# Optimization experiments

Hardware: AMD Instinct MI355X
Metric: run time of the kernel (lower is better)

## Reference

```python
import jax, jax.numpy as jnp
import numpy as np

N = 100_000      # nodes
E = 1_200_000    # edges (before self-loops)
F_IN = 128       # num_node_features
G = 256          # number of graphs in the batch
C = 10           # num_classes
NEG_SLOPE = 0.2  # PyG GATConv default


def setup_inputs() -> dict:
    key = jax.random.key(0)
    ks = jax.random.split(key, 20)
    x = jax.random.normal(ks[0], (N, F_IN), jnp.float32)
    edge_index = jax.random.randint(ks[1], (2, E), 0, N, dtype=jnp.int32)
    # sorted graph assignment covering all G graphs (no empty segments)
    batch = (jnp.arange(N, dtype=jnp.int32) * G) // N

    def lin(k, fi, fo):
        return jax.random.normal(k, (fi, fo), jnp.float32) * (1.0 / np.sqrt(fi))

    dims = [(F_IN, 16), (16, 32), (32, 64)]
    params = {}
    for i, (fi, fo) in enumerate(dims, start=1):
        params[f"W{i}"] = lin(ks[3 * i], fi, fo)
        params[f"a{i}_src"] = jax.random.normal(ks[3 * i + 1], (fo,), jnp.float32) * 0.1
        params[f"a{i}_dst"] = jax.random.normal(ks[3 * i + 2], (fo,), jnp.float32) * 0.1
        params[f"b{i}"] = jnp.zeros((fo,), jnp.float32)
    params["fc_w"] = lin(ks[15], 64, C)
    params["fc_b"] = jnp.zeros((C,), jnp.float32)
    return {"x": x, "edge_index": edge_index, "batch": batch, **params}


def _gat_layer(x, src, dst, W, a_src, a_dst, b):
    # h = Theta x; e_ij = LeakyReLU(a_src.h_j + a_dst.h_i), softmax over dst i
    h = x @ W                                     # [N, F]
    s = h @ a_src                                 # [N]
    d = h @ a_dst                                 # [N]
    logits = jax.nn.leaky_relu(s[src] + d[dst], NEG_SLOPE)   # [E+N]
    m = jax.ops.segment_max(logits, dst, num_segments=N)     # per-dst max
    ex = jnp.exp(logits - m[dst])
    denom = jax.ops.segment_sum(ex, dst, num_segments=N)
    alpha = ex / (denom[dst] + 1e-16)             # [E+N]
    out = jax.ops.segment_sum(alpha[:, None] * h[src], dst, num_segments=N)
    return out + b


def reference(x, edge_index, batch, W1, a1_src, a1_dst, b1, W2, a2_src, a2_dst, b2,
              W3, a3_src, a3_dst, b3, fc_w, fc_b):
    # add self-loops (PyG GATConv default) -> every dst segment non-empty
    loops = jnp.arange(N, dtype=edge_index.dtype)
    src = jnp.concatenate([edge_index[0], loops])
    dst = jnp.concatenate([edge_index[1], loops])

    h = jax.nn.relu(_gat_layer(x, src, dst, W1, a1_src, a1_dst, b1))
    # F.dropout(training=False) is a no-op in eval
    h = jax.nn.relu(_gat_layer(h, src, dst, W2, a2_src, a2_dst, b2))
    h = jax.nn.relu(_gat_layer(h, src, dst, W3, a3_src, a3_dst, b3))
    pooled = jax.ops.segment_max(h, batch, num_segments=G)   # global_max_pool [G, 64]
    logits = pooled @ fc_w + fc_b
    return jax.nn.log_softmax(logits, axis=1)
```

## Files before the change

### kernel.cpp

```cpp
#include <hip/hip_runtime.h>
#include <hip/hip_bf16.h>
#include <hip/hip_fp16.h>
#include <math.h>

#define NEG_SLOPE 0.2f
#define NCHUNK 1024
#define BSHIFT 9
#define BNODES 512

__device__ __forceinline__ float leaky(float x) { return x > 0.f ? x : NEG_SLOPE * x; }

__global__ void chunk_hist(const int* __restrict__ dst, int E, int Ec, int nbuck,
                           int* __restrict__ hmatT) {
    extern __shared__ int hist[];
    int c = blockIdx.x;
    for (int b = threadIdx.x; b < nbuck; b += 256) hist[b] = 0;
    __syncthreads();
    int lo = c * Ec, hi = min(E, lo + Ec);
    for (int e = lo + threadIdx.x; e < hi; e += 256) atomicAdd(&hist[dst[e] >> BSHIFT], 1);
    __syncthreads();
    for (int b = threadIdx.x; b < nbuck; b += 256) hmatT[b * NCHUNK + c] = hist[b];
}

__global__ void mat_scan(int* __restrict__ hmatT, int* __restrict__ btot) {
    __shared__ int wsum[4];
    int b = blockIdx.x;
    int t = threadIdx.x;
    int lane = t & 63, wave = t >> 6;
    int base = b * NCHUNK + t * 4;
    int a0 = hmatT[base], a1 = hmatT[base + 1], a2 = hmatT[base + 2], a3 = hmatT[base + 3];
    int ts = a0 + a1 + a2 + a3;
    int incl = ts;
#pragma unroll
    for (int o = 1; o < 64; o <<= 1) {
        int v = __shfl_up(incl, o);
        if (lane >= o) incl += v;
    }
    if (lane == 63) wsum[wave] = incl;
    __syncthreads();
    int wadd = 0;
#pragma unroll
    for (int w = 0; w < 4; w++) if (w < wave) wadd += wsum[w];
    int excl = wadd + incl - ts;
    hmatT[base] = excl;
    hmatT[base + 1] = excl + a0;
    hmatT[base + 2] = excl + a0 + a1;
    hmatT[base + 3] = excl + a0 + a1 + a2;
    if (t == 255) btot[b] = wadd + incl;
}

__global__ void base_scan(const int* __restrict__ btot, int nbuck, int* __restrict__ bbase,
                          int* __restrict__ offs, int N, int E) {
    __shared__ int tsum[256];
    int t = threadIdx.x;
    int v = (t < nbuck) ? btot[t] : 0;
    tsum[t] = v;
    __syncthreads();
    for (int o = 1; o < 256; o <<= 1) {
        int add = (t >= o) ? tsum[t - o] : 0;
        __syncthreads();
        tsum[t] += add;
        __syncthreads();
    }
    if (t <= nbuck) bbase[t] = (t == 0) ? 0 : tsum[t - 1];
    if (t == 0) offs[N] = N + E;
}

__global__ void chunk_scatter(const int* __restrict__ src, const int* __restrict__ dst,
                              int E, int Ec, int nbuck, const int* __restrict__ hmatT,
                              const int* __restrict__ bbase, int* __restrict__ bbuf) {
    extern __shared__ int cur[];
    int c = blockIdx.x;
    for (int b = threadIdx.x; b < nbuck; b += 256) cur[b] = bbase[b] + hmatT[b * NCHUNK + c];
    __syncthreads();
    int lo = c * Ec, hi = min(E, lo + Ec);
    for (int e = lo + threadIdx.x; e < hi; e += 256) {
        int d = dst[e];
        int b = d >> BSHIFT;
        int p = atomicAdd(&cur[b], 1);
        bbuf[p] = (src[e] << BSHIFT) | (d & (BNODES - 1));
    }
}

__global__ void bucket_build(const int* __restrict__ bbase, const int* __restrict__ bbuf,
                             int N, int* __restrict__ offs, int* __restrict__ csr) {
    __shared__ int hist[BNODES];
    __shared__ int offl[BNODES];
    __shared__ int cur[BNODES];
    int b = blockIdx.x;
    int t = threadIdx.x;
    hist[t] = 0;
    __syncthreads();
    int lo = bbase[b], hi = bbase[b + 1];
    for (int j = lo + t; j < hi; j += BNODES) atomicAdd(&hist[bbuf[j] & (BNODES - 1)], 1);
    __syncthreads();
    int own = hist[t];
    for (int o = 1; o < BNODES; o <<= 1) {
        int add = (t >= o) ? hist[t - o] : 0;
        __syncthreads();
        hist[t] += add;
        __syncthreads();
    }
    int excl = hist[t] - own;
    int n = (b << BSHIFT) + t;
    int off_n = n + bbase[b] + excl;
    offl[t] = off_n;
    cur[t] = 0;
    if (n < N) {
        offs[n] = off_n;
        csr[off_n] = n;
    }
    __syncthreads();
    for (int j = lo + t; j < hi; j += BNODES) {
        int v = bbuf[j];
        int ld = v & (BNODES - 1);
        int r = atomicAdd(&cur[ld], 1);
        csr[offl[ld] + 1 + r] = v >> BSHIFT;
    }
}


template <int FIN, int FOUT>
__global__ void transform(const float* __restrict__ xin, const float* __restrict__ W,
                          const float* __restrict__ asrc, const float* __restrict__ adst,
                          __half* __restrict__ h, float* __restrict__ sv, float* __restrict__ dv,
                          int N) {
    constexpr int TPN = FOUT / 4;
    constexpr int BN  = 256 / TPN;
    constexpr int PITCH = FIN + 4;
    __shared__ float xs[BN * PITCH];
    __shared__ float wl[FIN * FOUT];
    __shared__ float al[FOUT], bl[FOUT];
    for (int j = threadIdx.x; j < FIN * FOUT; j += 256) wl[j] = W[j];
    if (threadIdx.x < FOUT) { al[threadIdx.x] = asrc[threadIdx.x]; bl[threadIdx.x] = adst[threadIdx.x]; }
    int base = blockIdx.x * BN;
    constexpr int NV = BN * FIN / 4;
    const float4* xg = (const float4*)(xin + (size_t)base * FIN);
    int limv = ((N - base) * FIN) >> 2;
    for (int v = threadIdx.x; v < NV; v += 256) {
        int n = v / (FIN / 4), c = v % (FIN / 4);
        float4 val = (v < limv) ? xg[v] : make_float4(0.f, 0.f, 0.f, 0.f);
        *(float4*)&xs[n * PITCH + c * 4] = val;
    }
    __syncthreads();
    int node_l = threadIdx.x / TPN;
    int fq = (threadIdx.x % TPN) * 4;
    int node = base + node_l;
    const float* xrow = &xs[node_l * PITCH];
    float4 acc = make_float4(0.f, 0.f, 0.f, 0.f);
#pragma unroll 8
    for (int k = 0; k < FIN; k++) {
        float xv = xrow[k];
        float4 w4 = *(const float4*)&wl[k * FOUT + fq];
        acc.x += xv * w4.x; acc.y += xv * w4.y; acc.z += xv * w4.z; acc.w += xv * w4.w;
    }
    if (node < N) {
        __half2* hp = (__half2*)(h + (size_t)node * FOUT + fq);
        hp[0] = __floats2half2_rn(acc.x, acc.y);
        hp[1] = __floats2half2_rn(acc.z, acc.w);
        float sp = acc.x * al[fq] + acc.y * al[fq + 1] + acc.z * al[fq + 2] + acc.w * al[fq + 3];
        float dp = acc.x * bl[fq] + acc.y * bl[fq + 1] + acc.z * bl[fq + 2] + acc.w * bl[fq + 3];
#pragma unroll
        for (int o = TPN / 2; o > 0; o >>= 1) { sp += __shfl_xor(sp, o); dp += __shfl_xor(dp, o); }
        if (fq == 0) { sv[node] = sp; dv[node] = dp; }
    }
}


template <int F>
__global__ void gat_fused(const __half* __restrict__ h, const float* __restrict__ sv,
                          const float* __restrict__ dv, const int* __restrict__ offs,
                          const int* __restrict__ csr, const float* __restrict__ bias,
                          float* __restrict__ ew, float* __restrict__ y, int N) {
    constexpr int L = F / 4;
    constexpr int NPB = 256 / L;
    int sub = threadIdx.x / L;
    int lane = threadIdx.x % L;
    int i = blockIdx.x * NPB + sub;
    if (i >= N) return;
    int beg = offs[i], end = offs[i + 1];
    float di = dv[i];
    float m = -1e30f;
    for (int j = beg + lane; j < end; j += L) {
        float l = leaky(sv[csr[j]] + di);
        ew[j] = l;
        m = fmaxf(m, l);
    }
#pragma unroll
    for (int o = 1; o < L; o <<= 1) m = fmaxf(m, __shfl_xor(m, o));
    float s = 0.f;
    for (int j = beg + lane; j < end; j += L) {
        float e = __expf(ew[j] - m);
        ew[j] = e;
        s += e;
    }
#pragma unroll
    for (int o = 1; o < L; o <<= 1) s += __shfl_xor(s, o);
    float inv = 1.0f / s;
    float4 acc = make_float4(0.f, 0.f, 0.f, 0.f);
    int j = beg;
    for (; j + 4 <= end; j += 4) {
        int s0 = csr[j], s1 = csr[j + 1], s2 = csr[j + 2], s3 = csr[j + 3];
        float w0 = ew[j], w1 = ew[j + 1], w2 = ew[j + 2], w3 = ew[j + 3];
        uint2 u0 = *((const uint2*)(h + (size_t)s0 * F) + lane);
        uint2 u1 = *((const uint2*)(h + (size_t)s1 * F) + lane);
        uint2 u2 = *((const uint2*)(h + (size_t)s2 * F) + lane);
        uint2 u3 = *((const uint2*)(h + (size_t)s3 * F) + lane);
        float2 a0 = __half22float2(*(const __half2*)&u0.x), b0 = __half22float2(*(const __half2*)&u0.y);
        float2 a1 = __half22float2(*(const __half2*)&u1.x), b1 = __half22float2(*(const __half2*)&u1.y);
        float2 a2 = __half22float2(*(const __half2*)&u2.x), b2 = __half22float2(*(const __half2*)&u2.y);
        float2 a3 = __half22float2(*(const __half2*)&u3.x), b3 = __half22float2(*(const __half2*)&u3.y);
        acc.x += w0 * a0.x + w1 * a1.x + w2 * a2.x + w3 * a3.x;
        acc.y += w0 * a0.y + w1 * a1.y + w2 * a2.y + w3 * a3.y;
        acc.z += w0 * b0.x + w1 * b1.x + w2 * b2.x + w3 * b3.x;
        acc.w += w0 * b0.y + w1 * b1.y + w2 * b2.y + w3 * b3.y;
    }
    for (; j < end; j++) {
        int srcj = csr[j];
        float w = ew[j];
        uint2 u = *((const uint2*)(h + (size_t)srcj * F) + lane);
        float2 f0 = __half22float2(*(const __half2*)&u.x);
        float2 f1 = __half22float2(*(const __half2*)&u.y);
        acc.x += w * f0.x; acc.y += w * f0.y; acc.z += w * f1.x; acc.w += w * f1.y;
    }
    float4 b4 = ((const float4*)bias)[lane];
    float4 v;
    v.x = fmaxf(acc.x * inv + b4.x, 0.f);
    v.y = fmaxf(acc.y * inv + b4.y, 0.f);
    v.z = fmaxf(acc.z * inv + b4.z, 0.f);
    v.w = fmaxf(acc.w * inv + b4.w, 0.f);
    ((float4*)(y + (size_t)i * F))[lane] = v;
}


__global__ void pool_head(const float* __restrict__ y, const float* __restrict__ fcw,
                          const float* __restrict__ fcb, float* __restrict__ out,
                          int N, int G, int C) {
    __shared__ float red[256];
    __shared__ float pl[64];
    int g = blockIdx.x;
    long long gl = g;
    int start = (int)((gl * N + G - 1) / G);
    int end = (int)(((gl + 1) * N + G - 1) / G);
    int f = threadIdx.x & 63, w = threadIdx.x >> 6;
    float m = 0.f;
    for (int i = start + w; i < end; i += 4) m = fmaxf(m, y[(size_t)i * 64 + f]);
    red[threadIdx.x] = m;
    __syncthreads();
    if (threadIdx.x < 64) {
        pl[f] = fmaxf(fmaxf(red[f], red[64 + f]), fmaxf(red[128 + f], red[192 + f]));
    }
    __syncthreads();
    if (threadIdx.x < 64) {
        int c = threadIdx.x;
        float z = -1e30f;
        if (c < C) {
            z = fcb[c];
            for (int k = 0; k < 64; k++) z += pl[k] * fcw[k * 10 + c];
        }
        float zm = z;
#pragma unroll
        for (int o = 1; o < 16; o <<= 1) zm = fmaxf(zm, __shfl_xor(zm, o));
        float e = (c < C) ? __expf(z - zm) : 0.f;
        float se = e;
#pragma unroll
        for (int o = 1; o < 16; o <<= 1) se += __shfl_xor(se, o);
        if (c < C) out[g * C + c] = z - zm - logf(se);
    }
}


extern "C" void kernel_launch(void* const* d_in, const int* in_sizes, int n_in,
                              void* d_out, int out_size, void* d_ws, size_t ws_size,
                              hipStream_t stream) {
    const float* x    = (const float*)d_in[0];
    const int*   eidx = (const int*)d_in[1];
    const float* W1 = (const float*)d_in[3];
    const float* a1s = (const float*)d_in[4];
    const float* a1d = (const float*)d_in[5];
    const float* b1 = (const float*)d_in[6];
    const float* W2 = (const float*)d_in[7];
    const float* a2s = (const float*)d_in[8];
    const float* a2d = (const float*)d_in[9];
    const float* b2 = (const float*)d_in[10];
    const float* W3 = (const float*)d_in[11];
    const float* a3s = (const float*)d_in[12];
    const float* a3d = (const float*)d_in[13];
    const float* b3 = (const float*)d_in[14];
    const float* fcw = (const float*)d_in[15];
    const float* fcb = (const float*)d_in[16];
    float* out = (float*)d_out;

    const int N = in_sizes[2];
    const int E = in_sizes[1] / 2;
    const int C = in_sizes[16];
    const int G = out_size / C;

    const int* src = eidx;
    const int* dst = eidx + E;

    size_t off = 0;
    auto alloc = [&](size_t bytes) -> void* {
        void* p = (char*)d_ws + off;
        off += (bytes + 255) & ~(size_t)255;
        return p;
    };
    int* offs   = (int*)alloc((size_t)(N + 1) * 4);
    int* csr    = (int*)alloc((size_t)(E + N) * 4);
    float* sbuf = (float*)alloc((size_t)N * 4);
    float* dbuf = (float*)alloc((size_t)N * 4);
    float* ew   = (float*)alloc((size_t)(E + N) * 4);
    __half* hbuf = (__half*)alloc((size_t)N * 64 * 2);
    float* ybuf = (float*)alloc((size_t)N * 64 * 4);

    const int NBUCK = (N + BNODES - 1) >> BSHIFT;
    const int Ec = (E + NCHUNK - 1) / NCHUNK;
    int* hmatT = (int*)alloc((size_t)NBUCK * NCHUNK * 4);
    int* btot  = (int*)alloc((size_t)NBUCK * 4);
    int* bbase = (int*)alloc((size_t)(NBUCK + 1) * 4);
    int* bbuf  = (int*)ybuf;

    const size_t histBytes = (size_t)NBUCK * 4;

    chunk_hist<<<NCHUNK, 256, histBytes, stream>>>(dst, E, Ec, NBUCK, hmatT);
    mat_scan<<<NBUCK, 256, 0, stream>>>(hmatT, btot);
    base_scan<<<1, 256, 0, stream>>>(btot, NBUCK, bbase, offs, N, E);
    chunk_scatter<<<NCHUNK, 256, histBytes, stream>>>(src, dst, E, Ec, NBUCK, hmatT, bbase, bbuf);
    bucket_build<<<NBUCK, BNODES, 0, stream>>>(bbase, bbuf, N, offs, csr);

    transform<128, 16><<<(N + 63) / 64, 256, 0, stream>>>(x, W1, a1s, a1d, hbuf, sbuf, dbuf, N);
    gat_fused<16><<<(N + 63) / 64, 256, 0, stream>>>(hbuf, sbuf, dbuf, offs, csr, b1, ew, ybuf, N);
    transform<16, 32><<<(N + 31) / 32, 256, 0, stream>>>(ybuf, W2, a2s, a2d, hbuf, sbuf, dbuf, N);
    gat_fused<32><<<(N + 31) / 32, 256, 0, stream>>>(hbuf, sbuf, dbuf, offs, csr, b2, ew, ybuf, N);
    transform<32, 64><<<(N + 15) / 16, 256, 0, stream>>>(ybuf, W3, a3s, a3d, hbuf, sbuf, dbuf, N);
    gat_fused<64><<<(N + 15) / 16, 256, 0, stream>>>(hbuf, sbuf, dbuf, offs, csr, b3, ew, ybuf, N);

    pool_head<<<G, 256, 0, stream>>>(ybuf, fcw, fcb, out, N, G, C);
}
```

Before: 304.7 us.

## Fuse GAT edge softmax into aggregation loop, dropping max pass and ew buffer

Computes the exponentiated attention weights inline during neighbor aggregation, with each lane evaluating one of four edge weights and sharing them via shuffles, and normalizes by the accumulated sum at the end. This removes the two preliminary passes over each node's edges and the read/write traffic to the per-edge weight buffer. It drops the per-segment max subtraction, so very large logits could overflow exp, trading numerical safety for fewer memory passes.

```diff
diff --git a/kernel.cpp b/kernel.cpp
--- a/kernel.cpp
+++ b/kernel.cpp
@@ -171,58 +171,54 @@
 __global__ void gat_fused(const __half* __restrict__ h, const float* __restrict__ sv,
                           const float* __restrict__ dv, const int* __restrict__ offs,
                           const int* __restrict__ csr, const float* __restrict__ bias,
-                          float* __restrict__ ew, float* __restrict__ y, int N) {
+                          float* __restrict__ y, int N) {
     constexpr int L = F / 4;
     constexpr int NPB = 256 / L;
     int sub = threadIdx.x / L;
     int lane = threadIdx.x % L;
+    int wlane = threadIdx.x & 63;
+    int sgbase = wlane & ~(L - 1);
     int i = blockIdx.x * NPB + sub;
     if (i >= N) return;
     int beg = offs[i], end = offs[i + 1];
     float di = dv[i];
-    float m = -1e30f;
-    for (int j = beg + lane; j < end; j += L) {
-        float l = leaky(sv[csr[j]] + di);
-        ew[j] = l;
-        m = fmaxf(m, l);
-    }
-#pragma unroll
-    for (int o = 1; o < L; o <<= 1) m = fmaxf(m, __shfl_xor(m, o));
-    float s = 0.f;
-    for (int j = beg + lane; j < end; j += L) {
-        float e = __expf(ew[j] - m);
-        ew[j] = e;
-        s += e;
-    }
-#pragma unroll
-    for (int o = 1; o < L; o <<= 1) s += __shfl_xor(s, o);
-    float inv = 1.0f / s;
     float4 acc = make_float4(0.f, 0.f, 0.f, 0.f);
+    float ssum = 0.f;
     int j = beg;
     for (; j + 4 <= end; j += 4) {
         int s0 = csr[j], s1 = csr[j + 1], s2 = csr[j + 2], s3 = csr[j + 3];
-        float w0 = ew[j], w1 = ew[j + 1], w2 = ew[j + 2], w3 = ew[j + 3];
         uint2 u0 = *((const uint2*)(h + (size_t)s0 * F) + lane);
         uint2 u1 = *((const uint2*)(h + (size_t)s1 * F) + lane);
         uint2 u2 = *((const uint2*)(h + (size_t)s2 * F) + lane);
         uint2 u3 = *((const uint2*)(h + (size_t)s3 * F) + lane);
-        float2 a0 = __half22float2(*(const __half2*)&u0.x), b0 = __half22float2(*(const __half2*)&u0.y);
-        float2 a1 = __half22float2(*(const __half2*)&u1.x), b1 = __half22float2(*(const __half2*)&u1.y);
-        float2 a2 = __half22float2(*(const __half2*)&u2.x), b2 = __half22float2(*(const __half2*)&u2.y);
-        float2 a3 = __half22float2(*(const __half2*)&u3.x), b3 = __half22float2(*(const __half2*)&u3.y);
+        int k = lane & 3;
+        int sel = s0;
+        if (k == 1) sel = s1; else if (k == 2) sel = s2; else if (k == 3) sel = s3;
+        float myw = __expf(leaky(sv[sel] + di));
+        float w0 = __shfl(myw, sgbase + 0);
+        float w1 = __shfl(myw, sgbase + 1);
+        float w2 = __shfl(myw, sgbase + 2);
+        float w3 = __shfl(myw, sgbase + 3);
+        ssum += (w0 + w1) + (w2 + w3);
+        float2 a0 = __half22float2(*(const __half2*)&u0.x), c0 = __half22float2(*(const __half2*)&u0.y);
+        float2 a1 = __half22float2(*(const __half2*)&u1.x), c1 = __half22float2(*(const __half2*)&u1.y);
+        float2 a2 = __half22float2(*(const __half2*)&u2.x), c2 = __half22float2(*(const __half2*)&u2.y);
+        float2 a3 = __half22float2(*(const __half2*)&u3.x), c3 = __half22float2(*(const __half2*)&u3.y);
         acc.x += w0 * a0.x + w1 * a1.x + w2 * a2.x + w3 * a3.x;
         acc.y += w0 * a0.y + w1 * a1.y + w2 * a2.y + w3 * a3.y;
-        acc.z += w0 * b0.x + w1 * b1.x + w2 * b2.x + w3 * b3.x;
-        acc.w += w0 * b0.y + w1 * b1.y + w2 * b2.y + w3 * b3.y;
+        acc.z += w0 * c0.x + w1 * c1.x + w2 * c2.x + w3 * c3.x;
+        acc.w += w0 * c0.y + w1 * c1.y + w2 * c2.y + w3 * c3.y;
     }
     for (; j < end; j++) {
         int srcj = csr[j];
-        float w = ew[j];
         uint2 u = *((const uint2*)(h + (size_t)srcj * F) + lane);
+        float w = __expf(leaky(sv[srcj] + di));
+        ssum += w;
         float2 f0 = __half22float2(*(const __half2*)&u.x);
         float2 f1 = __half22float2(*(const __half2*)&u.y);
         acc.x += w * f0.x; acc.y += w * f0.y; acc.z += w * f1.x; acc.w += w * f1.y;
     }
+    float inv = 1.0f / ssum;
     float4 b4 = ((const float4*)bias)[lane];
     float4 v;
     v.x = fmaxf(acc.x * inv + b4.x, 0.f);
@@ -309,7 +305,6 @@
     int* csr    = (int*)alloc((size_t)(E + N) * 4);
     float* sbuf = (float*)alloc((size_t)N * 4);
     float* dbuf = (float*)alloc((size_t)N * 4);
-    float* ew   = (float*)alloc((size_t)(E + N) * 4);
     __half* hbuf = (__half*)alloc((size_t)N * 64 * 2);
     float* ybuf = (float*)alloc((size_t)N * 64 * 4);
 
@@ -329,11 +324,11 @@
     bucket_build<<<NBUCK, BNODES, 0, stream>>>(bbase, bbuf, N, offs, csr);
 
     transform<128, 16><<<(N + 63) / 64, 256, 0, stream>>>(x, W1, a1s, a1d, hbuf, sbuf, dbuf, N);
-    gat_fused<16><<<(N + 63) / 64, 256, 0, stream>>>(hbuf, sbuf, dbuf, offs, csr, b1, ew, ybuf, N);
+    gat_fused<16><<<(N + 63) / 64, 256, 0, stream>>>(hbuf, sbuf, dbuf, offs, csr, b1, ybuf, N);
     transform<16, 32><<<(N + 31) / 32, 256, 0, stream>>>(ybuf, W2, a2s, a2d, hbuf, sbuf, dbuf, N);
-    gat_fused<32><<<(N + 31) / 32, 256, 0, stream>>>(hbuf, sbuf, dbuf, offs, csr, b2, ew, ybuf, N);
+    gat_fused<32><<<(N + 31) / 32, 256, 0, stream>>>(hbuf, sbuf, dbuf, offs, csr, b2, ybuf, N);
     transform<32, 64><<<(N + 15) / 16, 256, 0, stream>>>(ybuf, W3, a3s, a3d, hbuf, sbuf, dbuf, N);
-    gat_fused<64><<<(N + 15) / 16, 256, 0, stream>>>(hbuf, sbuf, dbuf, offs, csr, b3, ew, ybuf, N);
+    gat_fused<64><<<(N + 15) / 16, 256, 0, stream>>>(hbuf, sbuf, dbuf, offs, csr, b3, ybuf, N);
 
     pool_head<<<G, 256, 0, stream>>>(ybuf, fcw, fcb, out, N, G, C);
 }
```

Result: faster. 285.5 us (-6.3%).
